# Kernel optimization log

Measured on AMD Instinct MI355X. Metric: run time of the kernel, lower is better.

The kernel has to match this reference:

```python
import jax, jax.numpy as jnp
import numpy as np
from jax import lax

THD = 0.8  # Lowe ratio-test threshold (module init kwarg `thd`)


def setup_inputs() -> dict:
    key = jax.random.key(0)
    k1, k2 = jax.random.split(key)
    desc1 = jax.random.normal(k1, (16384, 128), dtype=jnp.float32)
    desc2 = jax.random.normal(k2, (16384, 128), dtype=jnp.float32)
    return {"desc1": desc1, "desc2": desc2}


def _cdist(a, b):
    # Euclidean pairwise distances, (B1, B2), same math as torch.cdist(p=2)
    sq_a = jnp.sum(a * a, axis=-1, keepdims=True)          # (B1, 1)
    sq_b = jnp.sum(b * b, axis=-1)                          # (B2,)
    d2 = sq_a + sq_b - 2.0 * (a @ b.T)                      # (B1, B2)
    return jnp.sqrt(jnp.maximum(d2, 0.0))


def reference(desc1, desc2):
    cost = _cdist(desc1, desc2)                             # (B1, B2)
    # two smallest distances per row
    neg_vals, idxs_in_2 = lax.top_k(-cost, 2)               # (B1, 2) each
    vals = -neg_vals
    ratio = vals[:, 0] / vals[:, 1]                         # (B1,)
    mask = ratio <= THD                                     # (B1,) bool
    # jit-compatible padded outputs: masked-out rows carry 0 distance; the
    # boolean mask selects the valid (idxs_in1, idxs_in2) match rows, which is
    # the compaction torch does with boolean indexing.
    match_dists = jnp.where(mask, ratio, 0.0)               # (B1,)
    idxs_in1 = jnp.arange(desc1.shape[0], dtype=jnp.int32)
    matches_idxs = jnp.stack([idxs_in1, idxs_in_2[:, 0].astype(jnp.int32)], axis=1)  # (B1, 2)
    return match_dists, matches_idxs, mask
```

## Files before the change

### kernel.cpp

```cpp
#include <hip/hip_runtime.h>
#include <math.h>
#include <float.h>
#include <stdint.h>


typedef __attribute__((ext_vector_type(4))) float     f32x4;
typedef __attribute__((ext_vector_type(8))) _Float16  half8;

#define D_     128
#define BM_    256
#define BN_    32
#define CS_    8
#define PARTS_ 8

__device__ __forceinline__ void gload_lds16(const void* g, void* l) {
  auto gp = (const __attribute__((address_space(1))) unsigned int*)(uintptr_t)g;
  auto lp = (__attribute__((address_space(3))) unsigned int*)(uintptr_t)l;
  __builtin_amdgcn_global_load_lds(gp, lp, 16, 0, 0);
}

__global__ void norms_kernel(const float* __restrict__ d1,
                             const float* __restrict__ d2,
                             float* __restrict__ sq, int B) {
  int gid  = blockIdx.x * blockDim.x + threadIdx.x;
  int wid  = gid >> 6;
  int lane = gid & 63;
  if (wid >= 2 * B) return;
  const float* src = (wid < B) ? (d1 + (size_t)wid * D_)
                               : (d2 + (size_t)(wid - B) * D_);
  float2 v = ((const float2*)src)[lane];
  float s = fmaf(v.x, v.x, v.y * v.y);
  #pragma unroll
  for (int off = 32; off > 0; off >>= 1) s += __shfl_down(s, off, 64);
  if (lane == 0) sq[wid] = s;
}

__global__ void convert_kernel(const float* __restrict__ d1, const float* __restrict__ d2,
                               _Float16* __restrict__ Ahi, _Float16* __restrict__ Alo,
                               _Float16* __restrict__ BhiP, _Float16* __restrict__ BloP,
                               int B) {
  int i = blockIdx.x * blockDim.x + threadIdx.x;
  int total = B * 16;
  if (i >= 2 * total) return;
  bool isB = i >= total;
  int j    = isB ? i - total : i;
  int desc = j >> 4;
  int seg  = j & 15;
  const float* src = (isB ? d2 : d1) + (size_t)desc * D_ + seg * 8;
  float4 v0 = *(const float4*)(src);
  float4 v1 = *(const float4*)(src + 4);
  half8 hv, lv;
  float e[8] = {v0.x, v0.y, v0.z, v0.w, v1.x, v1.y, v1.z, v1.w};
  #pragma unroll
  for (int q = 0; q < 8; ++q) {
    _Float16 h = (_Float16)e[q];
    _Float16 l = (_Float16)(e[q] - (float)h);
    if (isB) { h = (_Float16)(-2.0f) * h; l = (_Float16)(-2.0f) * l; }
    hv[q] = h; lv[q] = l;
  }
  if (!isB) {
    *(half8*)(Ahi + (size_t)desc * D_ + seg * 8) = hv;
    *(half8*)(Alo + (size_t)desc * D_ + seg * 8) = lv;
  } else {
    int t   = desc >> 5, cloc = desc & 31;
    int nf  = cloc >> 4, c15  = cloc & 15;
    int kk  = seg >> 2,  gq   = seg & 3;
    size_t off = (size_t)t * 4096 + kk * 1024 + nf * 512 + gq * 128 + c15 * 8;
    *(half8*)(BhiP + off) = hv;
    *(half8*)(BloP + off) = lv;
  }
}

__global__ __launch_bounds__(256, 2)
void nn_mfma(const _Float16* __restrict__ Ahi, const _Float16* __restrict__ Alo,
             const _Float16* __restrict__ BhiP, const _Float16* __restrict__ BloP,
             const float* __restrict__ sqb,
             float* __restrict__ p_d0, float* __restrict__ p_d1,
             int* __restrict__ p_j0, int B) {
  extern __shared__ char smem[];
  const int tid  = threadIdx.x;
  const int lane = tid & 63;
  const int wid  = tid >> 6;
  const int l15  = lane & 15;
  const int g    = lane >> 4;

  const int nrb   = B / BM_;
  const int rb    = blockIdx.x % nrb;
  const int cspl  = blockIdx.x / nrb;
  const int i0    = rb * BM_;
  const int niter = (B / CS_) / BN_;
  const int tile0 = cspl * niter;

  half8 ah[4][4], al[4][4];
  #pragma unroll
  for (int mf = 0; mf < 4; ++mf) {
    int row = i0 + wid * 64 + mf * 16 + l15;
    const _Float16* pa = Ahi + (size_t)row * D_ + g * 8;
    const _Float16* pl = Alo + (size_t)row * D_ + g * 8;
    #pragma unroll
    for (int kk = 0; kk < 4; ++kk) {
      ah[mf][kk] = *(const half8*)(pa + kk * 32);
      al[mf][kk] = *(const half8*)(pl + kk * 32);
    }
  }

  const _Float16* srcW = ((wid < 2) ? BhiP : BloP)
                       + (size_t)tile0 * 4096 + (wid & 1) * 2048 + lane * 8;
  char* ldsW = smem + (wid >> 1) * 8192 + (wid & 1) * 4096;
  auto stage = [&](int bufbase, int it) {
    const _Float16* s = srcW + (size_t)it * 4096;
    char* l = ldsW + bufbase;
    #pragma unroll
    for (int e = 0; e < 4; ++e) gload_lds16(s + e * 512, l + e * 1024);
  };

  float best0[16], best1[16]; int bj[16];
  #pragma unroll
  for (int s = 0; s < 16; ++s) { best0[s] = FLT_MAX; best1[s] = FLT_MAX; bj[s] = 0x7fffffff; }

  float sjA[2], sjB[2];
  const int colg0 = tile0 * BN_ + l15;

  stage(0, 0);
  #pragma unroll
  for (int nf = 0; nf < 2; ++nf) sjA[nf] = sqb[colg0 + nf * 16];
  __syncthreads();

  auto body = [&](int it, int bufbase, float (&sjc)[2], float (&sjn)[2]) {
    if (it + 1 < niter) {
      stage(bufbase ^ 16384, it + 1);
      #pragma unroll
      for (int nf = 0; nf < 2; ++nf) sjn[nf] = sqb[colg0 + (it + 1) * BN_ + nf * 16];
    }

    f32x4 acc[4][2];
    __builtin_amdgcn_s_setprio(1);
    #pragma unroll
    for (int kk = 0; kk < 4; ++kk) {
      half8 bh[2], bl[2];
      #pragma unroll
      for (int nf = 0; nf < 2; ++nf) {
        bh[nf] = *(const half8*)(smem + bufbase + kk * 2048 + nf * 1024 + lane * 16);
        bl[nf] = *(const half8*)(smem + bufbase + 8192 + kk * 2048 + nf * 1024 + lane * 16);
      }
      #pragma unroll
      for (int mf = 0; mf < 4; ++mf)
        #pragma unroll
        for (int nf = 0; nf < 2; ++nf) {
          if (kk == 0) {
            f32x4 c0 = {sjc[nf], sjc[nf], sjc[nf], sjc[nf]};
            acc[mf][nf] = __builtin_amdgcn_mfma_f32_16x16x32_f16(ah[mf][0], bh[nf], c0, 0, 0, 0);
          } else {
            acc[mf][nf] = __builtin_amdgcn_mfma_f32_16x16x32_f16(ah[mf][kk], bh[nf], acc[mf][nf], 0, 0, 0);
          }
          acc[mf][nf] = __builtin_amdgcn_mfma_f32_16x16x32_f16(ah[mf][kk], bl[nf], acc[mf][nf], 0, 0, 0);
          acc[mf][nf] = __builtin_amdgcn_mfma_f32_16x16x32_f16(al[mf][kk], bh[nf], acc[mf][nf], 0, 0, 0);
        }
    }
    __builtin_amdgcn_s_setprio(0);

    #pragma unroll
    for (int nf = 0; nf < 2; ++nf) {
      int colg = colg0 + it * BN_ + nf * 16;
      #pragma unroll
      for (int mf = 0; mf < 4; ++mf)
        #pragma unroll
        for (int r = 0; r < 4; ++r) {
          int s = mf * 4 + r;
          float t = acc[mf][nf][r];
          bool lt0 = t < best0[s];
          best1[s] = fminf(best1[s], fmaxf(t, best0[s]));
          best0[s] = fminf(t, best0[s]);
          bj[s]    = lt0 ? colg : bj[s];
        }
    }
    __syncthreads();
  };

  for (int itp = 0; itp < niter; itp += 2) {
    body(itp,     0,     sjA, sjB);
    body(itp + 1, 16384, sjB, sjA);
  }

  #pragma unroll
  for (int off = 1; off < 16; off <<= 1) {
    #pragma unroll
    for (int s = 0; s < 16; ++s) {
      float e0 = __shfl_xor(best0[s], off, 64);
      float e1 = __shfl_xor(best1[s], off, 64);
      int   f0 = __shfl_xor(bj[s],    off, 64);
      if (e0 < best0[s] || (e0 == best0[s] && f0 < bj[s])) {
        best1[s] = fminf(best0[s], e1);
        best0[s] = e0;
        bj[s]    = f0;
      } else {
        best1[s] = fminf(best1[s], e0);
      }
    }
  }

  if (l15 == 0) {
    #pragma unroll
    for (int s = 0; s < 16; ++s) {
      int mf = s >> 2, r = s & 3;
      int row = i0 + wid * 64 + mf * 16 + g * 4 + r;
      p_d0[row * PARTS_ + cspl] = best0[s];
      p_d1[row * PARTS_ + cspl] = best1[s];
      p_j0[row * PARTS_ + cspl] = bj[s];
    }
  }
}

__global__ void nn_final(const float* __restrict__ sqa,
                         const float* __restrict__ p_d0,
                         const float* __restrict__ p_d1,
                         const int* __restrict__ p_j0,
                         float* __restrict__ out, int B) {
  int row = blockIdx.x * blockDim.x + threadIdx.x;
  if (row >= B) return;
  float d0 = FLT_MAX, d1 = FLT_MAX;
  int j0 = 0x7fffffff;
  for (int cs = 0; cs < PARTS_; ++cs) {
    float e0 = p_d0[row * PARTS_ + cs];
    float e1 = p_d1[row * PARTS_ + cs];
    int   f0 = p_j0[row * PARTS_ + cs];
    if (e0 < d0 || (e0 == d0 && f0 < j0)) {
      d1 = fminf(d0, e1);
      d0 = e0;
      j0 = f0;
    } else {
      d1 = fminf(d1, e0);
    }
  }
  float sa = sqa[row];
  float v0 = sqrtf(fmaxf(sa + d0, 0.f));
  float v1 = sqrtf(fmaxf(sa + d1, 0.f));
  float ratio = v0 / v1;
  bool m = (ratio <= 0.8f);
  out[row]             = m ? ratio : 0.f;
  out[B + row * 2]     = (float)row;
  out[B + row * 2 + 1] = (float)j0;
  out[3 * B + row]     = m ? 1.f : 0.f;
}

extern "C" void kernel_launch(void* const* d_in, const int* in_sizes, int n_in,
                              void* d_out, int out_size, void* d_ws, size_t ws_size,
                              hipStream_t stream) {
  const float* d1 = (const float*)d_in[0];
  const float* d2 = (const float*)d_in[1];
  const int B = in_sizes[0] / D_;

  float* ws   = (float*)d_ws;
  float* sqa  = ws;
  float* sqb  = ws + B;
  float* p_d0 = ws + 2 * B;
  float* p_d1 = ws + 10 * B;
  int*   p_j0 = (int*)(ws + 18 * B);
  _Float16* Ahi  = (_Float16*)(ws + 26 * B);
  _Float16* Alo  = Ahi + (size_t)B * D_;
  _Float16* BhiP = Alo + (size_t)B * D_;
  _Float16* BloP = BhiP + (size_t)B * D_;

  int nthreads = 2 * B * 64;
  norms_kernel<<<(nthreads + 255) / 256, 256, 0, stream>>>(d1, d2, sqa, B);

  int ngroups = 2 * B * 16;
  convert_kernel<<<(ngroups + 255) / 256, 256, 0, stream>>>(d1, d2, Ahi, Alo, BhiP, BloP, B);

  hipFuncSetAttribute((const void*)nn_mfma,
                      hipFuncAttributeMaxDynamicSharedMemorySize, 32768);
  nn_mfma<<<(B / BM_) * CS_, 256, 32768, stream>>>(Ahi, Alo, BhiP, BloP, sqb,
                                                   p_d0, p_d1, p_j0, B);

  nn_final<<<(B + 255) / 256, 256, 0, stream>>>(sqa, p_d0, p_d1, p_j0, (float*)d_out, B);
}
```

Before: 175.5 us.

## Software-pipeline top-2 fold one tile behind MFMA and reorder MFMA chains

Double-buffers the accumulators so the running top-2 update for the previous tile runs after the current tile's MFMAs are issued, letting VALU work overlap matrix-core latency. The three split-precision MFMA passes are regrouped so that dependent MFMAs on the same accumulator are spaced apart. best1 is now updated with a single med3 instruction instead of a min/max pair. This costs another 32 accumulator registers, which could reduce occupancy or cause spills. The first fold sees FLT_MAX placeholders, so its results are harmless.

```diff
diff --git a/kernel.cpp b/kernel.cpp
--- a/kernel.cpp
+++ b/kernel.cpp
@@ -118,22 +118,50 @@
   #pragma unroll
   for (int s = 0; s < 16; ++s) { best0[s] = FLT_MAX; best1[s] = FLT_MAX; bj[s] = 0x7fffffff; }
 
+  auto fold = [&](f32x4 (&a)[4][2], int colgBase) {
+    #pragma unroll
+    for (int nf = 0; nf < 2; ++nf) {
+      int colg = colgBase + nf * 16;
+      #pragma unroll
+      for (int mf = 0; mf < 4; ++mf)
+        #pragma unroll
+        for (int r = 0; r < 4; ++r) {
+          int s = mf * 4 + r;
+          float t = a[mf][nf][r];
+          best1[s] = __builtin_amdgcn_fmed3f(t, best0[s], best1[s]);
+          bool lt0 = t < best0[s];
+          best0[s] = fminf(t, best0[s]);
+          bj[s]    = lt0 ? colg : bj[s];
+        }
+    }
+  };
+
   float sjA[2], sjB[2];
   const int colg0 = tile0 * BN_ + l15;
 
+  f32x4 accA[4][2], accB[4][2];
+  #pragma unroll
+  for (int mf = 0; mf < 4; ++mf)
+    #pragma unroll
+    for (int nf = 0; nf < 2; ++nf) {
+      accA[mf][nf] = (f32x4){FLT_MAX, FLT_MAX, FLT_MAX, FLT_MAX};
+      accB[mf][nf] = (f32x4){FLT_MAX, FLT_MAX, FLT_MAX, FLT_MAX};
+    }
+
   stage(0, 0);
   #pragma unroll
   for (int nf = 0; nf < 2; ++nf) sjA[nf] = sqb[colg0 + nf * 16];
   __syncthreads();
 
-  auto body = [&](int it, int bufbase, float (&sjc)[2], float (&sjn)[2]) {
+  auto body = [&](int it, int bufbase,
+                  f32x4 (&accC)[4][2], f32x4 (&accP)[4][2],
+                  float (&sjc)[2], float (&sjn)[2]) {
     if (it + 1 < niter) {
       stage(bufbase ^ 16384, it + 1);
       #pragma unroll
       for (int nf = 0; nf < 2; ++nf) sjn[nf] = sqb[colg0 + (it + 1) * BN_ + nf * 16];
     }
 
-    f32x4 acc[4][2];
     __builtin_amdgcn_s_setprio(1);
     #pragma unroll
     for (int kk = 0; kk < 4; ++kk) {
@@ -149,38 +177,33 @@
         for (int nf = 0; nf < 2; ++nf) {
           if (kk == 0) {
             f32x4 c0 = {sjc[nf], sjc[nf], sjc[nf], sjc[nf]};
-            acc[mf][nf] = __builtin_amdgcn_mfma_f32_16x16x32_f16(ah[mf][0], bh[nf], c0, 0, 0, 0);
+            accC[mf][nf] = __builtin_amdgcn_mfma_f32_16x16x32_f16(ah[mf][0], bh[nf], c0, 0, 0, 0);
           } else {
-            acc[mf][nf] = __builtin_amdgcn_mfma_f32_16x16x32_f16(ah[mf][kk], bh[nf], acc[mf][nf], 0, 0, 0);
+            accC[mf][nf] = __builtin_amdgcn_mfma_f32_16x16x32_f16(ah[mf][kk], bh[nf], accC[mf][nf], 0, 0, 0);
           }
-          acc[mf][nf] = __builtin_amdgcn_mfma_f32_16x16x32_f16(ah[mf][kk], bl[nf], acc[mf][nf], 0, 0, 0);
-          acc[mf][nf] = __builtin_amdgcn_mfma_f32_16x16x32_f16(al[mf][kk], bh[nf], acc[mf][nf], 0, 0, 0);
         }
+      #pragma unroll
+      for (int mf = 0; mf < 4; ++mf)
+        #pragma unroll
+        for (int nf = 0; nf < 2; ++nf)
+          accC[mf][nf] = __builtin_amdgcn_mfma_f32_16x16x32_f16(ah[mf][kk], bl[nf], accC[mf][nf], 0, 0, 0);
+      #pragma unroll
+      for (int mf = 0; mf < 4; ++mf)
+        #pragma unroll
+        for (int nf = 0; nf < 2; ++nf)
+          accC[mf][nf] = __builtin_amdgcn_mfma_f32_16x16x32_f16(al[mf][kk], bh[nf], accC[mf][nf], 0, 0, 0);
     }
     __builtin_amdgcn_s_setprio(0);
 
-    #pragma unroll
-    for (int nf = 0; nf < 2; ++nf) {
-      int colg = colg0 + it * BN_ + nf * 16;
-      #pragma unroll
-      for (int mf = 0; mf < 4; ++mf)
-        #pragma unroll
-        for (int r = 0; r < 4; ++r) {
-          int s = mf * 4 + r;
-          float t = acc[mf][nf][r];
-          bool lt0 = t < best0[s];
-          best1[s] = fminf(best1[s], fmaxf(t, best0[s]));
-          best0[s] = fminf(t, best0[s]);
-          bj[s]    = lt0 ? colg : bj[s];
-        }
-    }
+    fold(accP, colg0 + (it - 1) * BN_);
     __syncthreads();
   };
 
   for (int itp = 0; itp < niter; itp += 2) {
-    body(itp,     0,     sjA, sjB);
-    body(itp + 1, 16384, sjB, sjA);
-  }
+    body(itp,     0,     accA, accB, sjA, sjB);
+    body(itp + 1, 16384, accB, accA, sjB, sjA);
+  }
+  fold(accB, colg0 + (niter - 1) * BN_);
 
   #pragma unroll
   for (int off = 1; off < 16; off <<= 1) {
```

After: 239.0 us. +36.2%, slower.
